# Kernel optimization log

Hardware: AMD Instinct MI355X
Metric: run time of the kernel (lower is better)

## Reference

```python
import jax, jax.numpy as jnp
import numpy as np

B, L, H = 4, 2048, 1024
NQ, NKV, D = 8, 2, 256
I, V = 3584, 16384
EPS = 1e-6
THETA = 1e7
ROPE_DIM = 64

def rmsnorm(x, w, eps=EPS):
    xf = x.astype(jnp.float32)
    rms = jax.lax.rsqrt(jnp.mean(xf * xf, axis=-1, keepdims=True) + eps)
    return (xf * rms).astype(x.dtype) * w

def apply_rope(x, positions):
    # x: [B, H, L, D]; rotate first ROPE_DIM dims, interleaved pairs
    n_pairs = ROPE_DIM // 2
    inv_freq = THETA ** (-2.0 * jnp.arange(n_pairs, dtype=jnp.float32) / ROPE_DIM)
    freqs = positions.astype(jnp.float32)[:, None] * inv_freq[None, :]  # [L, n_pairs]
    cos = jnp.cos(freqs)[None, None, :, :]
    sin = jnp.sin(freqs)[None, None, :, :]
    b, h, l, d = x.shape
    xr = x[..., :ROPE_DIM].reshape(b, h, l, n_pairs, 2)
    x0, x1 = xr[..., 0], xr[..., 1]
    r0 = x0 * cos - x1 * sin
    r1 = x0 * sin + x1 * cos
    rotated = jnp.stack([r0, r1], axis=-1).reshape(b, h, l, ROPE_DIM)
    return jnp.concatenate([rotated, x[..., ROPE_DIM:]], axis=-1)

def setup_inputs() -> dict:
    key = jax.random.key(0)
    ks = jax.random.split(key, 12)
    s = 0.02
    return {
        "embeddings": jax.random.normal(ks[0], (B, L, H), jnp.float32),
        "hidden_states": jax.random.normal(ks[1], (B, L, H), jnp.float32),
        "pre_emb_w": jnp.ones((H,), jnp.float32),
        "pre_hid_w": jnp.ones((H,), jnp.float32),
        "fc_w": jax.random.normal(ks[2], (H, 2 * H), jnp.float32) * s,
        "in_ln_w": jnp.ones((H,), jnp.float32),
        "q_w": jax.random.normal(ks[3], (2 * NQ * D, H), jnp.float32) * s,
        "k_w": jax.random.normal(ks[4], (NKV * D, H), jnp.float32) * s,
        "v_w": jax.random.normal(ks[5], (NKV * D, H), jnp.float32) * s,
        "o_w": jax.random.normal(ks[6], (H, NQ * D), jnp.float32) * s,
        "qn_w": jnp.ones((D,), jnp.float32),
        "kn_w": jnp.ones((D,), jnp.float32),
        "post_ln_w": jnp.ones((H,), jnp.float32),
        "gate_w": jax.random.normal(ks[7], (I, H), jnp.float32) * s,
        "up_w": jax.random.normal(ks[8], (I, H), jnp.float32) * s,
        "down_w": jax.random.normal(ks[9], (H, I), jnp.float32) * s,
        "norm_w": jnp.ones((H,), jnp.float32),
        "lm_w": jax.random.normal(ks[10], (V, H), jnp.float32) * s,
    }

def _attention(x, q_w, k_w, v_w, o_w, qn_w, kn_w):
    b, l, _ = x.shape
    qg = (x @ q_w.T).reshape(b, l, NQ, 2, D)
    q = qg[:, :, :, 0, :]
    gate = qg[:, :, :, 1, :]
    k = (x @ k_w.T).reshape(b, l, NKV, D)
    v = (x @ v_w.T).reshape(b, l, NKV, D)
    q = rmsnorm(q, qn_w)
    k = rmsnorm(k, kn_w)
    groups = NQ // NKV
    k = jnp.repeat(k, groups, axis=2)  # [B, L, NQ, D]
    v = jnp.repeat(v, groups, axis=2)
    q, k, v = (t.transpose(0, 2, 1, 3) for t in (q, k, v))  # [B, NQ, L, D]
    positions = jnp.arange(l)
    q = apply_rope(q, positions)
    k = apply_rope(k, positions)
    scores = jnp.einsum('bhqd,bhkd->bhqk', q, k) / jnp.sqrt(jnp.float32(D))
    causal = jnp.tril(jnp.ones((l, l), jnp.bool_))
    scores = jnp.where(causal[None, None], scores, jnp.finfo(scores.dtype).min)
    attn = jax.nn.softmax(scores, axis=-1)
    out = jnp.einsum('bhqk,bhkd->bhqd', attn, v)
    out = out.transpose(0, 2, 1, 3).reshape(b, l, NQ * D)
    out = out * jax.nn.sigmoid(gate.reshape(b, l, NQ * D))
    return out @ o_w.T

def reference(embeddings, hidden_states, pre_emb_w, pre_hid_w, fc_w, in_ln_w,
              q_w, k_w, v_w, o_w, qn_w, kn_w, post_ln_w, gate_w, up_w, down_w,
              norm_w, lm_w):
    x = jnp.concatenate([rmsnorm(embeddings, pre_emb_w),
                         rmsnorm(hidden_states, pre_hid_w)], axis=-1)
    x = x @ fc_w.T
    residual = x
    x = rmsnorm(x, in_ln_w)
    x = _attention(x, q_w, k_w, v_w, o_w, qn_w, kn_w)
    x = residual + x
    residual = x
    x = rmsnorm(x, post_ln_w)
    x = (jax.nn.silu(x @ gate_w.T) * (x @ up_w.T)) @ down_w.T
    x = residual + x
    x = rmsnorm(x, norm_w)
    return x @ lm_w.T
```

## Files before the change

### kernel.cpp

```cpp
#include <hip/hip_runtime.h>

typedef __bf16 bf16;
typedef __bf16 bf16x8 __attribute__((ext_vector_type(8)));
typedef __bf16 bf16x4 __attribute__((ext_vector_type(4)));
typedef float f32x4 __attribute__((ext_vector_type(4)));

__device__ inline f32x4 mfma16(bf16x8 a, bf16x8 b, f32x4 c) {
    return __builtin_amdgcn_mfma_f32_16x16x32_bf16(a, b, c, 0, 0, 0);
}

__device__ __forceinline__ void async_cp16(const void* g, void* l) {
    __builtin_amdgcn_global_load_lds(
        (__attribute__((address_space(1))) char*)g,
        (__attribute__((address_space(3))) char*)l,
        16, 0, 0);
}

__global__ __launch_bounds__(256) void w2b_kernel(const float* __restrict__ s,
                                                  bf16* __restrict__ d)
{
    const size_t i = ((size_t)blockIdx.x * 256 + threadIdx.x) * 4;
    const float4 f = *(const float4*)(s + i);
    bf16x4 t;
    t[0] = (bf16)f.x; t[1] = (bf16)f.y; t[2] = (bf16)f.z; t[3] = (bf16)f.w;
    *(bf16x4*)(d + i) = t;
}

template <int EPI>
__global__ __launch_bounds__(256) void gemm_kernel(
    const bf16* __restrict__ A, const bf16* __restrict__ B,
    const float* __restrict__ res, float* __restrict__ Cout,
    int M, int N, int K)
{
    __shared__ bf16 As[128 * 32];
    __shared__ bf16 Bs[128 * 32];
    const int tid = threadIdx.x;
    const int wave = tid >> 6, lane = tid & 63;
    const int quad = lane >> 4, l16 = lane & 15;

    const int nby = M >> 7, nbx = N >> 7;
    const int nwg = nbx * nby;
    int bid = blockIdx.x;
    {
        const int q = nwg >> 3, r = nwg & 7;
        const int x = bid & 7, loc = bid >> 3;
        bid = (x < r ? x * (q + 1) : r * (q + 1) + (x - r) * q) + loc;
    }
    const int pg = nbx << 3;
    const int g = bid / pg, rem = bid - g * pg;
    const int by = (g << 3) + (rem & 7);
    const int bx = rem >> 3;
    const int row0 = by << 7, col0 = bx << 7;
    const int wrow = ((wave >> 1) << 6), wcol = ((wave & 1) << 6);

    f32x4 acc[4][4] = {};

    const bf16* Ag = A + (size_t)(row0 + (tid >> 2)) * K + (tid & 3) * 8;
    const bf16* Bg = B + (size_t)(col0 + (tid >> 2)) * K + (tid & 3) * 8;
    bf16* Asw = As + wave * 512;
    bf16* Bsw = Bs + wave * 512;
    const size_t K64 = (size_t)64 * K;

    for (int kb = 0; kb < K; kb += 32) {
        async_cp16(Ag + kb,        Asw);
        async_cp16(Ag + K64 + kb,  Asw + 2048);
        async_cp16(Bg + kb,        Bsw);
        async_cp16(Bg + K64 + kb,  Bsw + 2048);
        __syncthreads();
        bf16x8 af[4], bfr[4];
#pragma unroll
        for (int i = 0; i < 4; ++i)
            af[i] = *(const bf16x8*)(&As[(wrow + i * 16 + l16) * 32 + quad * 8]);
#pragma unroll
        for (int j = 0; j < 4; ++j)
            bfr[j] = *(const bf16x8*)(&Bs[(wcol + j * 16 + l16) * 32 + quad * 8]);
#pragma unroll
        for (int i = 0; i < 4; ++i)
#pragma unroll
            for (int j = 0; j < 4; ++j)
                acc[i][j] = mfma16(af[i], bfr[j], acc[i][j]);
        __syncthreads();
    }

#pragma unroll
    for (int i = 0; i < 4; ++i) {
        const int row = row0 + wrow + i * 16 + quad * 4;
#pragma unroll
        for (int j = 0; j < 4; ++j) {
            const int col = col0 + wcol + j * 16 + l16;
#pragma unroll
            for (int r = 0; r < 4; ++r) {
                const size_t idx = (size_t)(row + r) * N + col;
                float v = acc[i][j][r];
                if (EPI == 1) Cout[idx] = v + res[idx];
                else          Cout[idx] = v;
            }
        }
    }
}

__global__ __launch_bounds__(256) void prenorm_kernel(
    const float* __restrict__ emb, const float* __restrict__ hid,
    const float* __restrict__ we, const float* __restrict__ wh,
    bf16* __restrict__ xcat)
{
    const int rr = blockIdx.x * 4 + (threadIdx.x >> 6);
    const int lane = threadIdx.x & 63;
    const int half = rr & 1, row = rr >> 1;
    const float* x = (half ? hid : emb) + (size_t)row * 1024;
    const float* w = half ? wh : we;
    float4 v[4]; float ss = 0.f;
#pragma unroll
    for (int j = 0; j < 4; ++j) {
        v[j] = *(const float4*)(x + (size_t)(lane + 64 * j) * 4);
        ss += v[j].x * v[j].x + v[j].y * v[j].y + v[j].z * v[j].z + v[j].w * v[j].w;
    }
#pragma unroll
    for (int m = 32; m; m >>= 1) ss += __shfl_xor(ss, m, 64);
    const float rms = rsqrtf(ss * (1.f / 1024.f) + 1e-6f);
    bf16* o = xcat + (size_t)row * 2048 + half * 1024;
#pragma unroll
    for (int j = 0; j < 4; ++j) {
        const int d = (lane + 64 * j) * 4;
        float4 wv = *(const float4*)(w + d);
        bf16x4 t;
        t[0] = (bf16)(v[j].x * rms * wv.x);
        t[1] = (bf16)(v[j].y * rms * wv.y);
        t[2] = (bf16)(v[j].z * rms * wv.z);
        t[3] = (bf16)(v[j].w * rms * wv.w);
        *(bf16x4*)(o + d) = t;
    }
}

__global__ __launch_bounds__(256) void rmsnorm_kernel(
    const float* __restrict__ xin, const float* __restrict__ w, bf16* __restrict__ out)
{
    const int row = blockIdx.x * 4 + (threadIdx.x >> 6);
    const int lane = threadIdx.x & 63;
    const float* x = xin + (size_t)row * 1024;
    float4 v[4]; float ss = 0.f;
#pragma unroll
    for (int j = 0; j < 4; ++j) {
        v[j] = *(const float4*)(x + (size_t)(lane + 64 * j) * 4);
        ss += v[j].x * v[j].x + v[j].y * v[j].y + v[j].z * v[j].z + v[j].w * v[j].w;
    }
#pragma unroll
    for (int m = 32; m; m >>= 1) ss += __shfl_xor(ss, m, 64);
    const float rms = rsqrtf(ss * (1.f / 1024.f) + 1e-6f);
    bf16* o = out + (size_t)row * 1024;
#pragma unroll
    for (int j = 0; j < 4; ++j) {
        const int d = (lane + 64 * j) * 4;
        float4 wv = *(const float4*)(w + d);
        bf16x4 t;
        t[0] = (bf16)(v[j].x * rms * wv.x);
        t[1] = (bf16)(v[j].y * rms * wv.y);
        t[2] = (bf16)(v[j].z * rms * wv.z);
        t[3] = (bf16)(v[j].w * rms * wv.w);
        *(bf16x4*)(o + d) = t;
    }
}

__global__ __launch_bounds__(256) void qprep_kernel(
    const float* __restrict__ qg, const float* __restrict__ qn_w, bf16* __restrict__ qa)
{
    const int row = blockIdx.x * 4 + (threadIdx.x >> 6);
    const int lane = threadIdx.x & 63;
    const int h = row & 7, bl = row >> 3;
    const int l = bl & 2047, b = bl >> 11;
    const float* x = qg + (size_t)row * 512;
    float v[4]; float ss = 0.f;
#pragma unroll
    for (int j = 0; j < 4; ++j) { v[j] = x[lane + 64 * j]; ss += v[j] * v[j]; }
#pragma unroll
    for (int m = 32; m; m >>= 1) ss += __shfl_xor(ss, m, 64);
    const float rms = rsqrtf(ss * (1.f / 256.f) + 1e-6f);
    float y[4];
#pragma unroll
    for (int j = 0; j < 4; ++j) y[j] = v[j] * rms * qn_w[lane + 64 * j];
    {
        const float p = __shfl_xor(y[0], 1, 64);
        const int i2 = lane >> 1;
        const float inv = powf(1e7f, -(float)(2 * i2) * (1.f / 64.f));
        const float ang = (float)l * inv;
        const float c = cosf(ang), s = sinf(ang);
        y[0] = (lane & 1) ? (p * s + y[0] * c) : (y[0] * c - p * s);
    }
    bf16* o = qa + ((size_t)((b * 8 + h) * 2048 + l)) * 256;
#pragma unroll
    for (int j = 0; j < 4; ++j) o[lane + 64 * j] = (bf16)(y[j] * 0.0625f);
}

__global__ __launch_bounds__(256) void kprep_kernel(
    const float* __restrict__ kf, const float* __restrict__ kn_w, bf16* __restrict__ ka)
{
    const int row = blockIdx.x * 4 + (threadIdx.x >> 6);
    const int lane = threadIdx.x & 63;
    const int kv = row & 1, bl = row >> 1;
    const int l = bl & 2047, b = bl >> 11;
    const float* x = kf + (size_t)row * 256;
    float v[4]; float ss = 0.f;
#pragma unroll
    for (int j = 0; j < 4; ++j) { v[j] = x[lane + 64 * j]; ss += v[j] * v[j]; }
#pragma unroll
    for (int m = 32; m; m >>= 1) ss += __shfl_xor(ss, m, 64);
    const float rms = rsqrtf(ss * (1.f / 256.f) + 1e-6f);
    float y[4];
#pragma unroll
    for (int j = 0; j < 4; ++j) y[j] = v[j] * rms * kn_w[lane + 64 * j];
    {
        const float p = __shfl_xor(y[0], 1, 64);
        const int i2 = lane >> 1;
        const float inv = powf(1e7f, -(float)(2 * i2) * (1.f / 64.f));
        const float ang = (float)l * inv;
        const float c = cosf(ang), s = sinf(ang);
        y[0] = (lane & 1) ? (p * s + y[0] * c) : (y[0] * c - p * s);
    }
    bf16* o = ka + ((size_t)((b * 2 + kv) * 2048 + l)) * 256;
#pragma unroll
    for (int j = 0; j < 4; ++j) o[lane + 64 * j] = (bf16)y[j];
}

__global__ __launch_bounds__(256) void vprep_kernel(const float* __restrict__ vf,
                                                    bf16* __restrict__ vt)
{
    __shared__ float t[64][65];
    const int l0 = blockIdx.x << 6;
    const int d0 = blockIdx.y << 6;
    const int b = blockIdx.z >> 1, kv = blockIdx.z & 1;
    const int tx = threadIdx.x & 63, ty = threadIdx.x >> 6;
    const float* src = vf + ((size_t)b * 4096 + kv) * 256;
#pragma unroll
    for (int j = 0; j < 16; ++j) {
        const int l = ty + j * 4;
        t[l][tx] = src[(size_t)(l0 + l) * 512 + d0 + tx];
    }
    __syncthreads();
    bf16* dst = vt + (size_t)(b * 2 + kv) * 256 * 2048;
#pragma unroll
    for (int j = 0; j < 16; ++j) {
        const int d = ty + j * 4;
        dst[(size_t)(d0 + d) * 2048 + l0 + tx] = (bf16)t[tx][d];
    }
}

__global__ __launch_bounds__(256) void attn_kernel(
    const bf16* __restrict__ qa, const bf16* __restrict__ ka,
    const bf16* __restrict__ vt, float* __restrict__ of)
{
    __shared__ bf16 Ks[32 * 264];
    __shared__ bf16 Vt[256 * 40];
    __shared__ bf16 Pw[4 * 16 * 40];
    const int tid = threadIdx.x;
    const int wave = tid >> 6, lane = tid & 63;
    const int quad = lane >> 4, l16 = lane & 15;
    const int bid = blockIdx.x;
    const int qt = bid & 31, h = (bid >> 5) & 7, b = bid >> 8;
    const int kvh = h >> 2;
    const bf16* qptr = qa + ((size_t)(b * 8 + h)) * 2048 * 256;
    const bf16* kptr = ka + ((size_t)(b * 2 + kvh)) * 2048 * 256;
    const bf16* vptr = vt + ((size_t)(b * 2 + kvh)) * 256 * 2048;
    const int qbase = qt * 64 + wave * 16;

    bf16x8 qf[8];
#pragma unroll
    for (int db = 0; db < 8; ++db)
        qf[db] = *(const bf16x8*)(qptr + (size_t)(qbase + l16) * 256 + db * 32 + quad * 8);

    f32x4 o_acc[16] = {};
    float m_i[4], l_i[4];
#pragma unroll
    for (int r = 0; r < 4; ++r) { m_i[r] = -1e30f; l_i[r] = 0.f; }

    const int ntiles = qt * 2 + 2;
    for (int kt = 0; kt < ntiles; ++kt) {
        const int kvs = kt * 32;
#pragma unroll
        for (int c = 0; c < 4; ++c) {
            const int idx = tid + c * 256;
            const int kr = idx >> 5, kc = (idx & 31) * 8;
            *(bf16x8*)(&Ks[kr * 264 + kc]) = *(const bf16x8*)(kptr + (size_t)(kvs + kr) * 256 + kc);
            const int vd = idx >> 2, vc = (idx & 3) * 8;
            *(bf16x8*)(&Vt[vd * 40 + vc]) = *(const bf16x8*)(vptr + (size_t)vd * 2048 + kvs + vc);
        }
        __syncthreads();

        f32x4 s0 = {}, s1 = {};
#pragma unroll
        for (int db = 0; db < 8; ++db) {
            bf16x8 k0 = *(const bf16x8*)(&Ks[l16 * 264 + db * 32 + quad * 8]);
            bf16x8 k1 = *(const bf16x8*)(&Ks[(16 + l16) * 264 + db * 32 + quad * 8]);
            s0 = mfma16(qf[db], k0, s0);
            s1 = mfma16(qf[db], k1, s1);
        }

        float alpha[4], p0v[4], p1v[4];
#pragma unroll
        for (int r = 0; r < 4; ++r) {
            const int qrow = qbase + quad * 4 + r;
            float a0 = (kvs + l16 > qrow) ? -1e30f : s0[r];
            float a1 = (kvs + 16 + l16 > qrow) ? -1e30f : s1[r];
            float mx = fmaxf(a0, a1);
#pragma unroll
            for (int m = 8; m; m >>= 1) mx = fmaxf(mx, __shfl_xor(mx, m, 64));
            const float mnew = fmaxf(m_i[r], mx);
            const float a = __expf(m_i[r] - mnew);
            const float p0 = __expf(a0 - mnew);
            const float p1 = __expf(a1 - mnew);
            float ps = p0 + p1;
#pragma unroll
            for (int m = 8; m; m >>= 1) ps += __shfl_xor(ps, m, 64);
            l_i[r] = l_i[r] * a + ps;
            m_i[r] = mnew;
            alpha[r] = a; p0v[r] = p0; p1v[r] = p1;
        }
#pragma unroll
        for (int t = 0; t < 16; ++t) {
            f32x4 o = o_acc[t];
            o[0] *= alpha[0]; o[1] *= alpha[1]; o[2] *= alpha[2]; o[3] *= alpha[3];
            o_acc[t] = o;
        }
        bf16* pw = &Pw[wave * 16 * 40];
#pragma unroll
        for (int r = 0; r < 4; ++r) {
            pw[(quad * 4 + r) * 40 + l16]      = (bf16)p0v[r];
            pw[(quad * 4 + r) * 40 + 16 + l16] = (bf16)p1v[r];
        }
        __syncthreads();
        const bf16x8 pa = *(const bf16x8*)(&pw[l16 * 40 + quad * 8]);
#pragma unroll
        for (int t = 0; t < 16; ++t) {
            bf16x8 vfr = *(const bf16x8*)(&Vt[(t * 16 + l16) * 40 + quad * 8]);
            o_acc[t] = mfma16(pa, vfr, o_acc[t]);
        }
        __syncthreads();
    }

    float* optr = of + ((size_t)(b * 8 + h)) * 2048 * 256;
#pragma unroll
    for (int r = 0; r < 4; ++r) {
        const float inv = 1.f / l_i[r];
        const int row = qbase + quad * 4 + r;
#pragma unroll
        for (int t = 0; t < 16; ++t)
            optr[(size_t)row * 256 + t * 16 + l16] = o_acc[t][r] * inv;
    }
}

__global__ void gating_kernel(const float* __restrict__ of, const float* __restrict__ qg,
                              bf16* __restrict__ ag)
{
    const size_t i = (size_t)blockIdx.x * 256 + threadIdx.x;
    const int d = (int)(i & 255);
    const int h = (int)((i >> 8) & 7);
    const size_t bl = i >> 11;
    const float o = of[((size_t)((bl >> 11) * 8 + h) * 2048 + (bl & 2047)) * 256 + d];
    const float g = qg[(bl * 8 + h) * 512 + 256 + d];
    ag[i] = (bf16)(o * (1.f / (1.f + __expf(-g))));
}

__global__ void silu_kernel(const float* __restrict__ g, const float* __restrict__ u,
                            bf16* __restrict__ h)
{
    const size_t i = ((size_t)blockIdx.x * 256 + threadIdx.x) * 4;
    const float4 gv = *(const float4*)(g + i);
    const float4 uv = *(const float4*)(u + i);
    bf16x4 t;
    t[0] = (bf16)(gv.x * (1.f / (1.f + __expf(-gv.x))) * uv.x);
    t[1] = (bf16)(gv.y * (1.f / (1.f + __expf(-gv.y))) * uv.y);
    t[2] = (bf16)(gv.z * (1.f / (1.f + __expf(-gv.z))) * uv.z);
    t[3] = (bf16)(gv.w * (1.f / (1.f + __expf(-gv.w))) * uv.w);
    *(bf16x4*)(h + i) = t;
}

extern "C" void kernel_launch(void* const* d_in, const int* in_sizes, int n_in,
                              void* d_out, int out_size, void* d_ws, size_t ws_size,
                              hipStream_t stream)
{
    const float* emb       = (const float*)d_in[0];
    const float* hid       = (const float*)d_in[1];
    const float* pre_emb_w = (const float*)d_in[2];
    const float* pre_hid_w = (const float*)d_in[3];
    const float* fc_w      = (const float*)d_in[4];
    const float* in_ln_w   = (const float*)d_in[5];
    const float* q_w       = (const float*)d_in[6];
    const float* k_w       = (const float*)d_in[7];
    const float* v_w       = (const float*)d_in[8];
    const float* o_w       = (const float*)d_in[9];
    const float* qn_w      = (const float*)d_in[10];
    const float* kn_w      = (const float*)d_in[11];
    const float* post_ln_w = (const float*)d_in[12];
    const float* gate_w    = (const float*)d_in[13];
    const float* up_w      = (const float*)d_in[14];
    const float* down_w    = (const float*)d_in[15];
    const float* norm_w    = (const float*)d_in[16];
    const float* lm_w      = (const float*)d_in[17];
    float* out = (float*)d_out;
    char* ws = (char*)d_ws;

    float* xres = (float*)(ws + 0);
    bf16*  xln  = (bf16*)(ws + 33554432);
    char*  C    = ws + 50331648;
    char*  D    = ws + 184549376;
    char*  E    = ws + 318767104;
    float* qg   = (float*)C;
    float* gf   = (float*)C;
    bf16*  xcat = (bf16*)D;
    float* kf   = (float*)(D + 33554432);
    float* vf   = (float*)(D + 50331648);
    float* of   = (float*)(D + 67108864);
    float* uf   = (float*)D;
    bf16*  qa   = (bf16*)E;
    bf16*  ka   = (bf16*)(E + 33554432);
    bf16*  va   = (bf16*)(E + 41943040);
    bf16*  ag   = (bf16*)E;
    bf16*  hb   = (bf16*)E;
    bf16*  wbC  = (bf16*)C;
    bf16*  wbD  = (bf16*)D;
    bf16*  wbDt = (bf16*)(D + 117440512);

    prenorm_kernel<<<4096, 256, 0, stream>>>(emb, hid, pre_emb_w, pre_hid_w, xcat);

    w2b_kernel<<<2048, 256, 0, stream>>>(fc_w, wbC);
    gemm_kernel<0><<<512, 256, 0, stream>>>(xcat, wbC, nullptr, xres, 8192, 1024, 2048);
    rmsnorm_kernel<<<2048, 256, 0, stream>>>(xres, in_ln_w, xln);

    w2b_kernel<<<4096, 256, 0, stream>>>(q_w, wbD);
    gemm_kernel<0><<<2048, 256, 0, stream>>>(xln, wbD, nullptr, qg, 8192, 4096, 1024);
    w2b_kernel<<<512, 256, 0, stream>>>(k_w, wbD);
    gemm_kernel<0><<<256, 256, 0, stream>>>(xln, wbD, nullptr, kf, 8192, 512, 1024);
    w2b_kernel<<<512, 256, 0, stream>>>(v_w, wbD);
    gemm_kernel<0><<<256, 256, 0, stream>>>(xln, wbD, nullptr, vf, 8192, 512, 1024);

    qprep_kernel<<<16384, 256, 0, stream>>>(qg, qn_w, qa);
    kprep_kernel<<<4096, 256, 0, stream>>>(kf, kn_w, ka);
    vprep_kernel<<<dim3(32, 4, 8), 256, 0, stream>>>(vf, va);
    attn_kernel<<<1024, 256, 0, stream>>>(qa, ka, va, of);
    gating_kernel<<<65536, 256, 0, stream>>>(of, qg, ag);

    w2b_kernel<<<2048, 256, 0, stream>>>(o_w, wbC);
    gemm_kernel<1><<<512, 256, 0, stream>>>(ag, wbC, xres, xres, 8192, 1024, 2048);
    rmsnorm_kernel<<<2048, 256, 0, stream>>>(xres, post_ln_w, xln);

    w2b_kernel<<<3584, 256, 0, stream>>>(gate_w, wbDt);
    gemm_kernel<0><<<1792, 256, 0, stream>>>(xln, wbDt, nullptr, gf, 8192, 3584, 1024);
    w2b_kernel<<<3584, 256, 0, stream>>>(up_w, wbDt);
    gemm_kernel<0><<<1792, 256, 0, stream>>>(xln, wbDt, nullptr, uf, 8192, 3584, 1024);
    silu_kernel<<<28672, 256, 0, stream>>>(gf, uf, hb);

    w2b_kernel<<<3584, 256, 0, stream>>>(down_w, wbC);
    gemm_kernel<1><<<512, 256, 0, stream>>>(hb, wbC, xres, xres, 8192, 1024, 3584);
    rmsnorm_kernel<<<2048, 256, 0, stream>>>(xres, norm_w, xln);

    w2b_kernel<<<16384, 256, 0, stream>>>(lm_w, wbC);
    gemm_kernel<0><<<8192, 256, 0, stream>>>(xln, wbC, nullptr, out, 8192, 16384, 1024);
}
```

Baseline: 2.105 ms.

## Add 256x256-tile pipelined GEMM kernel for large projections and LM head

Adds a new 512-thread GEMM that computes 256x256 output tiles with XOR-swizzled LDS, double-buffered async global-to-LDS loads and interleaved MFMA quadrants under setprio. It also remaps workgroup IDs for better cache locality. The kernel is used for the Q/gate projection, the gate and up MLP projections and the LM head. The aim is higher arithmetic intensity and better overlap of loads with MFMAs than the 128-tile kernel gives. In exchange it needs more registers and LDS per block and only works when M and N are multiples of 256.

Measured after the change: 1.954 ms. 7.2% less time.

```diff
diff --git a/kernel.cpp b/kernel.cpp
--- a/kernel.cpp
+++ b/kernel.cpp
@@ -92,6 +92,146 @@
             for (int r = 0; r < 4; ++r) {
                 const size_t idx = (size_t)(row + r) * N + col;
                 float v = acc[i][j][r];
+                if (EPI == 1) Cout[idx] = v + res[idx];
+                else          Cout[idx] = v;
+            }
+        }
+    }
+}
+
+template <int EPI>
+__global__ __launch_bounds__(512, 2) void gemm256_kernel(
+    const bf16* __restrict__ A, const bf16* __restrict__ B,
+    const float* __restrict__ res, float* __restrict__ Cout,
+    int M, int N, int K)
+{
+    __shared__ bf16 As[2][2][128][64];
+    __shared__ bf16 Bs[2][2][128][64];
+    const int tid = threadIdx.x;
+    const int wid = tid >> 6, lane = tid & 63;
+    const int quad = lane >> 4, l16 = lane & 15;
+    const int wm = wid >> 2, wn = wid & 3;
+    const int xsw = l16 & 7;
+
+    const int nby = M >> 8, nbx = N >> 8;
+    const int nwg = nbx * nby;
+    int bid = blockIdx.x;
+    {
+        const int q = nwg >> 3, r = nwg & 7;
+        const int x = bid & 7, loc = bid >> 3;
+        bid = (x < r ? x * (q + 1) : r * (q + 1) + (x - r) * q) + loc;
+    }
+    const int pg = nbx << 3;
+    const int g = bid / pg, rem = bid - g * pg;
+    const int by = (g << 3) + (rem & 7);
+    const int bx = rem >> 3;
+    const int row0 = by << 8, col0 = bx << 8;
+
+    const int srow = tid >> 3;
+    const int scol = ((tid & 7) ^ ((tid >> 3) & 7)) * 8;
+    const bf16* Abase = A + (size_t)(row0 + srow) * K + scol;
+    const bf16* Bbase = B + (size_t)(col0 + srow) * K + scol;
+    const size_t K64 = (size_t)K * 64;
+    const size_t K128 = (size_t)K * 128;
+
+    f32x4 acc[8][4] = {};
+
+#define STG_A(BUF, HH, KB) do { \
+    const bf16* _g = Abase + (size_t)(HH) * K128 + (KB); \
+    bf16* _l = &As[BUF][HH][0][0] + wid * 512; \
+    async_cp16(_g, _l); \
+    async_cp16(_g + K64, _l + 4096); } while (0)
+#define STG_B(BUF, HH, KB) do { \
+    const bf16* _g = Bbase + (size_t)(HH) * K128 + (KB); \
+    bf16* _l = &Bs[BUF][HH][0][0] + wid * 512; \
+    async_cp16(_g, _l); \
+    async_cp16(_g + K64, _l + 4096); } while (0)
+
+#define READ_A(RH) do { \
+    _Pragma("unroll") for (int f = 0; f < 4; ++f) { \
+        af[f*2+0] = *(const bf16x8*)(&Ah[(RH)*64 + f*16 + l16][(quad ^ xsw) * 8]); \
+        af[f*2+1] = *(const bf16x8*)(&Ah[(RH)*64 + f*16 + l16][((4 + quad) ^ xsw) * 8]); } } while (0)
+
+#define READ_B(CH, BF) do { \
+    _Pragma("unroll") for (int f = 0; f < 2; ++f) { \
+        BF[f*2+0] = *(const bf16x8*)(&Bh[bofs + (CH)*32 + f*16 + l16][(quad ^ xsw) * 8]); \
+        BF[f*2+1] = *(const bf16x8*)(&Bh[bofs + (CH)*32 + f*16 + l16][((4 + quad) ^ xsw) * 8]); } } while (0)
+
+#define MFMA_Q(RH, CH, BF) do { \
+    _Pragma("unroll") for (int f = 0; f < 4; ++f) \
+    _Pragma("unroll") for (int f2 = 0; f2 < 2; ++f2) { \
+        acc[(RH)*4+f][(CH)*2+f2] = mfma16(af[f*2+0], BF[f2*2+0], acc[(RH)*4+f][(CH)*2+f2]); \
+        acc[(RH)*4+f][(CH)*2+f2] = mfma16(af[f*2+1], BF[f2*2+1], acc[(RH)*4+f][(CH)*2+f2]); } } while (0)
+
+    const int NT = K >> 6;
+    STG_B(0, 0, 0); STG_B(0, 1, 0); STG_A(0, 0, 0); STG_A(0, 1, 0);
+    if (NT > 1) {
+        STG_B(1, 0, 64); STG_B(1, 1, 64); STG_A(1, 0, 64);
+        asm volatile("s_waitcnt vmcnt(6)" ::: "memory");
+    } else {
+        asm volatile("s_waitcnt vmcnt(0)" ::: "memory");
+    }
+    __builtin_amdgcn_s_barrier();
+
+    bf16x8 af[8], bf0[4], bf1[4];
+    for (int t = 0; t < NT; ++t) {
+        const int c = t & 1, n = c ^ 1;
+        const bf16 (*Ah)[64] = As[c][wm];
+        const bf16 (*Bh)[64] = Bs[c][wn >> 1];
+        const int bofs = (wn & 1) * 64;
+        const int kb1 = (t + 1) << 6, kb2 = (t + 2) << 6;
+        READ_A(0); READ_B(0, bf0);
+        if (t + 1 < NT) STG_A(n, 1, kb1);
+        __builtin_amdgcn_s_barrier();
+        asm volatile("s_waitcnt lgkmcnt(0)" ::: "memory");
+        __builtin_amdgcn_sched_barrier(0);
+        __builtin_amdgcn_s_setprio(1);
+        MFMA_Q(0, 0, bf0);
+        __builtin_amdgcn_s_setprio(0);
+        __builtin_amdgcn_s_barrier();
+        READ_B(1, bf1);
+        if (t + 2 < NT) STG_B(c, 0, kb2);
+        __builtin_amdgcn_s_barrier();
+        asm volatile("s_waitcnt lgkmcnt(0)" ::: "memory");
+        __builtin_amdgcn_sched_barrier(0);
+        __builtin_amdgcn_s_setprio(1);
+        MFMA_Q(0, 1, bf1);
+        __builtin_amdgcn_s_setprio(0);
+        __builtin_amdgcn_s_barrier();
+        READ_A(1);
+        if (t + 2 < NT) STG_B(c, 1, kb2);
+        __builtin_amdgcn_s_barrier();
+        asm volatile("s_waitcnt lgkmcnt(0)" ::: "memory");
+        __builtin_amdgcn_sched_barrier(0);
+        __builtin_amdgcn_s_setprio(1);
+        MFMA_Q(1, 0, bf0);
+        __builtin_amdgcn_s_setprio(0);
+        __builtin_amdgcn_s_barrier();
+        if (t + 2 < NT) STG_A(c, 0, kb2);
+        __builtin_amdgcn_s_barrier();
+        __builtin_amdgcn_s_setprio(1);
+        MFMA_Q(1, 1, bf1);
+        __builtin_amdgcn_s_setprio(0);
+        if (t + 2 < NT)      { asm volatile("s_waitcnt vmcnt(6)" ::: "memory"); }
+        else if (t + 1 < NT) { asm volatile("s_waitcnt vmcnt(0)" ::: "memory"); }
+        __builtin_amdgcn_s_barrier();
+    }
+#undef STG_A
+#undef STG_B
+#undef READ_A
+#undef READ_B
+#undef MFMA_Q
+
+#pragma unroll
+    for (int fr = 0; fr < 8; ++fr) {
+        const int row = row0 + wm * 128 + fr * 16 + quad * 4;
+#pragma unroll
+        for (int fc = 0; fc < 4; ++fc) {
+            const int col = col0 + wn * 64 + fc * 16 + l16;
+#pragma unroll
+            for (int r = 0; r < 4; ++r) {
+                const size_t idx = (size_t)(row + r) * N + col;
+                float v = acc[fr][fc][r];
                 if (EPI == 1) Cout[idx] = v + res[idx];
                 else          Cout[idx] = v;
             }
@@ -426,7 +566,7 @@
     rmsnorm_kernel<<<2048, 256, 0, stream>>>(xres, in_ln_w, xln);
 
     w2b_kernel<<<4096, 256, 0, stream>>>(q_w, wbD);
-    gemm_kernel<0><<<2048, 256, 0, stream>>>(xln, wbD, nullptr, qg, 8192, 4096, 1024);
+    gemm256_kernel<0><<<512, 512, 0, stream>>>(xln, wbD, nullptr, qg, 8192, 4096, 1024);
     w2b_kernel<<<512, 256, 0, stream>>>(k_w, wbD);
     gemm_kernel<0><<<256, 256, 0, stream>>>(xln, wbD, nullptr, kf, 8192, 512, 1024);
     w2b_kernel<<<512, 256, 0, stream>>>(v_w, wbD);
@@ -443,9 +583,9 @@
     rmsnorm_kernel<<<2048, 256, 0, stream>>>(xres, post_ln_w, xln);
 
     w2b_kernel<<<3584, 256, 0, stream>>>(gate_w, wbDt);
-    gemm_kernel<0><<<1792, 256, 0, stream>>>(xln, wbDt, nullptr, gf, 8192, 3584, 1024);
+    gemm256_kernel<0><<<448, 512, 0, stream>>>(xln, wbDt, nullptr, gf, 8192, 3584, 1024);
     w2b_kernel<<<3584, 256, 0, stream>>>(up_w, wbDt);
-    gemm_kernel<0><<<1792, 256, 0, stream>>>(xln, wbDt, nullptr, uf, 8192, 3584, 1024);
+    gemm256_kernel<0><<<448, 512, 0, stream>>>(xln, wbDt, nullptr, uf, 8192, 3584, 1024);
     silu_kernel<<<28672, 256, 0, stream>>>(gf, uf, hb);
 
     w2b_kernel<<<3584, 256, 0, stream>>>(down_w, wbC);
@@ -453,5 +593,5 @@
     rmsnorm_kernel<<<2048, 256, 0, stream>>>(xres, norm_w, xln);
 
     w2b_kernel<<<16384, 256, 0, stream>>>(lm_w, wbC);
-    gemm_kernel<0><<<8192, 256, 0, stream>>>(xln, wbC, nullptr, out, 8192, 16384, 1024);
-}
+    gemm256_kernel<0><<<2048, 512, 0, stream>>>(xln, wbC, nullptr, out, 8192, 16384, 1024);
+}
```
